# Kernel tuning notes

Measured on AMD Instinct MI355X. Metric: run time of the kernel, lower is better.

The kernel has to match this reference:

```python
import jax, jax.numpy as jnp
import numpy as np

EPS = 1e-5

def conv3d(x, w, b):
    y = jax.lax.conv_general_dilated(x, w, (1, 1, 1), [(1, 1), (1, 1), (1, 1)],
                                     dimension_numbers=('NCDHW', 'OIDHW', 'NCDHW'))
    return y + b[None, :, None, None, None]

def batchnorm(x, g, b):
    # training-mode BN: biased batch statistics over (N, D, H, W)
    m = jnp.mean(x, axis=(0, 2, 3, 4), keepdims=True)
    v = jnp.mean((x - m) ** 2, axis=(0, 2, 3, 4), keepdims=True)
    return (x - m) * jax.lax.rsqrt(v + EPS) * g[None, :, None, None, None] + b[None, :, None, None, None]

def deform_conv3d(x, offset, w, b):
    # x: (B,C,D,H,W); offset: (B, 3*27, D,H,W); w: (O,C,3,3,3)
    B, C, D, H, W = x.shape
    N = 27
    xp = jnp.pad(x, ((0, 0), (0, 0), (1, 1), (1, 1), (1, 1)))
    Dp, Hp, Wp = D + 2, H + 2, W + 2
    off = offset.reshape(B, 3, N, D, H, W)
    kk = jnp.arange(3, dtype=x.dtype) - 1.0  # kernel taps -1,0,1
    kd, kh, kw = [a.reshape(-1) for a in jnp.meshgrid(kk, kk, kk, indexing='ij')]
    # sampling positions in padded coords: p0 (=out idx + pad) + kernel tap + learned offset
    pd = jnp.clip((jnp.arange(D, dtype=x.dtype) + 1.0)[None, None, :, None, None]
                  + kd[None, :, None, None, None] + off[:, 0], 0.0, Dp - 1)
    ph = jnp.clip((jnp.arange(H, dtype=x.dtype) + 1.0)[None, None, None, :, None]
                  + kh[None, :, None, None, None] + off[:, 1], 0.0, Hp - 1)
    pw = jnp.clip((jnp.arange(W, dtype=x.dtype) + 1.0)[None, None, None, None, :]
                  + kw[None, :, None, None, None] + off[:, 2], 0.0, Wp - 1)
    q0d = jnp.clip(jnp.floor(pd), 0, Dp - 2); td = jnp.clip(pd - q0d, 0.0, 1.0)
    q0h = jnp.clip(jnp.floor(ph), 0, Hp - 2); th = jnp.clip(ph - q0h, 0.0, 1.0)
    q0w = jnp.clip(jnp.floor(pw), 0, Wp - 2); tw = jnp.clip(pw - q0w, 0.0, 1.0)
    q0d = q0d.astype(jnp.int32); q0h = q0h.astype(jnp.int32); q0w = q0w.astype(jnp.int32)
    xf = xp.reshape(B, C, -1)
    acc = jnp.zeros((B, C, N, D, H, W), dtype=x.dtype)
    for i in (0, 1):
        for j in (0, 1):
            for k in (0, 1):
                idx = ((q0d + i) * Hp + (q0h + j)) * Wp + (q0w + k)  # (B,N,D,H,W)
                g = ((td if i else 1.0 - td) * (th if j else 1.0 - th) * (tw if k else 1.0 - tw))
                gath = jnp.take_along_axis(xf, idx.reshape(B, 1, -1), axis=2).reshape(B, C, N, D, H, W)
                acc = acc + g[:, None] * gath
    out = jnp.einsum('bcndhw,ocn->bodhw', acc, w.reshape(w.shape[0], C, N))
    return out + b[None, :, None, None, None]


def setup_inputs() -> dict:
    ks = jax.random.split(jax.random.key(0), 16)
    s = 0.05
    f32 = jnp.float32
    return {
        'x': jax.random.normal(ks[0], (4, 1, 28, 28, 8), f32),
        'c1w': jax.random.normal(ks[1], (32, 1, 3, 3, 3), f32) * s, 'c1b': jnp.zeros((32,), f32),
        'g1': jnp.ones((32,), f32), 'b1': jnp.zeros((32,), f32),
        'c2w': jax.random.normal(ks[2], (64, 32, 3, 3, 3), f32) * s, 'c2b': jnp.zeros((64,), f32),
        'g2': jnp.ones((64,), f32), 'b2': jnp.zeros((64,), f32),
        'c3w': jax.random.normal(ks[3], (128, 64, 3, 3, 3), f32) * s, 'c3b': jnp.zeros((128,), f32),
        'g3': jnp.ones((128,), f32), 'b3': jnp.zeros((128,), f32),
        'ow': jax.random.normal(ks[4], (81, 128, 3, 3, 3), f32) * s, 'ob': jnp.zeros((81,), f32),
        'dw': jax.random.normal(ks[5], (128, 128, 3, 3, 3), f32) * s, 'db': jnp.zeros((128,), f32),
        'g4': jnp.ones((128,), f32), 'b4': jnp.zeros((128,), f32),
        'fcw': jax.random.normal(ks[6], (10, 128), f32) * s, 'fcb': jnp.zeros((10,), f32),
    }


def reference(x, c1w, c1b, g1, b1, c2w, c2b, g2, b2, c3w, c3b, g3, b3,
              ow, ob, dw, db, g4, b4, fcw, fcb):
    h = batchnorm(jax.nn.relu(conv3d(x, c1w, c1b)), g1, b1)
    h = batchnorm(jax.nn.relu(conv3d(h, c2w, c2b)), g2, b2)
    h = batchnorm(jax.nn.relu(conv3d(h, c3w, c3b)), g3, b3)
    offsets = conv3d(h, ow, ob)
    h = batchnorm(jax.nn.relu(deform_conv3d(h, offsets, dw, db)), g4, b4)
    pooled = jnp.mean(h, axis=(2, 3, 4))  # avg_pool over full (28,28,d) extent
    logits = pooled @ fcw.T + fcb
    return jax.nn.log_softmax(logits, axis=1), offsets
```

## Files before the change

kernel.cpp:

```cpp
#include <hip/hip_runtime.h>
#include <math.h>

#define BB 4
#define SP 6272
#define NSP 25088
#define EPS 1e-5f

typedef unsigned short u16;
typedef __attribute__((ext_vector_type(8))) short v8s;
typedef __attribute__((ext_vector_type(4))) float v4f;

__device__ __forceinline__ u16 f2b(float f) {
    unsigned u = __float_as_uint(f);
    return (u16)((u + 0x7fffu + ((u >> 16) & 1u)) >> 16);
}
__device__ __forceinline__ float b2f(u16 s) {
    return __uint_as_float(((unsigned)s) << 16);
}
__device__ __forceinline__ float b2f_lo(unsigned x) { return __uint_as_float(x << 16); }
__device__ __forceinline__ float b2f_hi(unsigned x) { return __uint_as_float(x & 0xffff0000u); }

__global__ __launch_bounds__(256) __attribute__((amdgpu_waves_per_eu(1, 4)))
void conv1_shfl(const float* __restrict__ X, const float* __restrict__ Wt,
                const float* __restrict__ bias, u16* __restrict__ Ybf,
                float* __restrict__ s_sum, float* __restrict__ s_sq)
{
    const int OT = 16;
    __shared__ float red[4][32];
    int xblk = blockIdx.x;
    int sblk = (xblk & 7) * 13 + (xblk >> 3);
    if (sblk >= 98) return;
    int t = threadIdx.x;
    int s = sblk * 256 + t;
    int b = s / SP;
    int sp = s - b * SP;
    int d = sp / 224;
    int r = sp - d * 224;
    int h = r >> 3;
    int w = r & 7;
    int o0 = blockIdx.y * OT;

    float mdh[9]; int odh[9];
    #pragma unroll
    for (int i = 0; i < 3; i++) {
        int dd = d + i - 1;
        float md = ((unsigned)dd < 28u) ? 1.f : 0.f;
        int ddc = min(max(dd, 0), 27);
        #pragma unroll
        for (int j = 0; j < 3; j++) {
            int hh = h + j - 1;
            float mh = ((unsigned)hh < 28u) ? 1.f : 0.f;
            int hhc = min(max(hh, 0), 27);
            mdh[i * 3 + j] = md * mh;
            odh[i * 3 + j] = ddc * 224 + hhc * 8 + w;
        }
    }
    float mw0 = (w > 0) ? 1.f : 0.f;
    float mw2 = (w < 7) ? 1.f : 0.f;

    float acc[OT];
    #pragma unroll
    for (int oo = 0; oo < OT; oo++) acc[oo] = bias[o0 + oo];

    const float* xc = X + (size_t)b * SP;
    #pragma unroll
    for (int t9 = 0; t9 < 9; t9++) {
        float x0 = xc[odh[t9]];
        float m = mdh[t9];
        float xm = __shfl_up(x0, 1, 64) * (m * mw0);
        float xz = x0 * m;
        float xp = __shfl_down(x0, 1, 64) * (m * mw2);
        #pragma unroll
        for (int oo = 0; oo < OT; oo++) {
            const float* wp = Wt + (size_t)(o0 + oo) * 27 + t9 * 3;
            acc[oo] = fmaf(xm, wp[0], acc[oo]);
            acc[oo] = fmaf(xz, wp[1], acc[oo]);
            acc[oo] = fmaf(xp, wp[2], acc[oo]);
        }
    }
    float sv[OT];
    #pragma unroll
    for (int oo = 0; oo < OT; oo++) sv[oo] = fmaxf(acc[oo], 0.f);

    unsigned pk[8];
    #pragma unroll
    for (int j = 0; j < 8; j++)
        pk[j] = (unsigned)f2b(sv[2 * j]) | ((unsigned)f2b(sv[2 * j + 1]) << 16);
    u16* row = Ybf + (size_t)(b * SP + sp) * 32 + o0;
    *(uint4*)(row)     = make_uint4(pk[0], pk[1], pk[2], pk[3]);
    *(uint4*)(row + 8) = make_uint4(pk[4], pk[5], pk[6], pk[7]);

    int l = t & 63, wvv = t >> 6;
    #pragma unroll
    for (int oo = 0; oo < OT; oo++) {
        float ss = sv[oo], qv = ss * ss;
        #pragma unroll
        for (int m = 1; m < 64; m <<= 1) {
            ss += __shfl_xor(ss, m, 64);
            qv += __shfl_xor(qv, m, 64);
        }
        if (l == 0) { red[wvv][oo] = ss; red[wvv][16 + oo] = qv; }
    }
    __syncthreads();
    if (t < 32) {
        float tot = red[0][t] + red[1][t] + red[2][t] + red[3][t];
        if (t < 16) atomicAdd(&s_sum[o0 + t], tot);
        else        atomicAdd(&s_sq[o0 + t - 16], tot);
    }
}

__global__ __launch_bounds__(256) void prepack_all(const float* __restrict__ c2w,
        const float* __restrict__ c3w, const float* __restrict__ ow,
        const float* __restrict__ dw, u16* __restrict__ wpk2,
        u16* __restrict__ wpk3, u16* __restrict__ wpko, u16* __restrict__ dwa,
        float* __restrict__ ws0)
{
    int bx = blockIdx.x;
    if (bx >= 4536) {
        int i = (bx - 4536) * 256 + threadIdx.x;
        if (i < 2048) ws0[i] = 0.f;
        return;
    }
    int idx = bx * 256 + threadIdx.x;
    if (idx < 55296) {
        int t = idx / 2048, rem = idx & 2047, o = rem >> 5, c = rem & 31;
        wpk2[idx] = f2b(c2w[((size_t)o * 32 + c) * 27 + t]);
    } else if (idx < 276480) {
        int i = idx - 55296;
        int t = i / 8192, rem = i & 8191, o = rem >> 6, c = rem & 63;
        wpk3[i] = f2b(c3w[((size_t)o * 64 + c) * 27 + t]);
    } else if (idx < 718848) {
        int i = idx - 276480;
        int t = i / 16384, rem = i & 16383, o = rem >> 7, c = rem & 127;
        wpko[i] = f2b((o < 81) ? ow[((size_t)o * 128 + c) * 27 + t] : 0.f);
    } else {
        int i = idx - 718848;
        int j = i & 7, r = (i >> 3) & 15, q = (i >> 7) & 3;
        int kc = (i >> 9) & 3, ot = (i >> 11) & 7, n = i >> 14;
        int o = ot * 16 + r, c = kc * 32 + q * 8 + j;
        dwa[i] = f2b(dw[((size_t)o * 128 + c) * 27 + n]);
    }
}

template<int CIN, int OPAD, bool OFFOUT, bool BNIN>
__global__ __launch_bounds__(256) __attribute__((amdgpu_waves_per_eu(1, 4)))
void conv_mfma(const u16* __restrict__ X, const u16* __restrict__ Wpk,
               const float* __restrict__ bias, u16* __restrict__ Ybf,
               float* __restrict__ offs, float* __restrict__ s_sum,
               float* __restrict__ s_sq, const float* __restrict__ in_sum,
               const float* __restrict__ in_sq, const float* __restrict__ in_g,
               const float* __restrict__ in_b)
{
    const int HS = CIN + 8;
    __shared__ u16 xs[160 * HS];
    __shared__ float scin[BNIN ? CIN : 1], shin[BNIN ? CIN : 1];

    int tid = threadIdx.x;
    int fid = blockIdx.x;
    int g = (fid & 7) * 98 + (fid >> 3);
    int b = g / 196;
    int rem = g - b * 196;
    int d0 = (rem / 14) * 2, h0 = (rem % 14) * 2;

    if (BNIN) {
        if (tid < CIN) {
            float m = in_sum[tid] * (1.f / NSP);
            float v = in_sq[tid] * (1.f / NSP) - m * m;
            float sc = in_g[tid] * rsqrtf(v + EPS);
            scin[tid] = sc;
            shin[tid] = in_b[tid] - m * sc;
        }
        __syncthreads();
    }

    const int NCH = CIN / 8;
    for (int idx = tid; idx < 160 * NCH; idx += 256) {
        int pos = idx / NCH, ch = idx - pos * NCH;
        int dz = pos / 40, r2 = pos - dz * 40;
        int hz = r2 / 10, wz = r2 - hz * 10;
        int dd = d0 + dz - 1, hh = h0 + hz - 1, ww = wz - 1;
        uint4 val = make_uint4(0, 0, 0, 0);
        if ((unsigned)dd < 28u && (unsigned)hh < 28u && (unsigned)ww < 8u) {
            val = *(const uint4*)(X + ((size_t)(b * SP + dd * 224 + hh * 8 + ww) * CIN + ch * 8));
            if (BNIN) {
                int cb = ch * 8;
                float f0 = b2f_lo(val.x) * scin[cb]     + shin[cb];
                float f1 = b2f_hi(val.x) * scin[cb + 1] + shin[cb + 1];
                float f2 = b2f_lo(val.y) * scin[cb + 2] + shin[cb + 2];
                float f3 = b2f_hi(val.y) * scin[cb + 3] + shin[cb + 3];
                float f4 = b2f_lo(val.z) * scin[cb + 4] + shin[cb + 4];
                float f5 = b2f_hi(val.z) * scin[cb + 5] + shin[cb + 5];
                float f6 = b2f_lo(val.w) * scin[cb + 6] + shin[cb + 6];
                float f7 = b2f_hi(val.w) * scin[cb + 7] + shin[cb + 7];
                val.x = (unsigned)f2b(f0) | ((unsigned)f2b(f1) << 16);
                val.y = (unsigned)f2b(f2) | ((unsigned)f2b(f3) << 16);
                val.z = (unsigned)f2b(f4) | ((unsigned)f2b(f5) << 16);
                val.w = (unsigned)f2b(f6) | ((unsigned)f2b(f7) << 16);
            }
        }
        *(uint4*)(xs + pos * HS + ch * 8) = val;
    }
    __syncthreads();

    int l = tid & 63, wv = tid >> 6;
    int q = l >> 4, r = l & 15;
    int hl = r >> 3, wl = r & 7;

    if (OFFOUT && blockIdx.y == 1) {
        int dl = wv >> 1;
        int o = 64 + ((wv & 1) << 4) + r;
        const u16* ap = xs + ((4 + hl + 1) * 10 + wl + 1) * HS + 8 * q + dl * 40 * HS;
        const u16* wp0 = Wpk + (size_t)o * CIN + 8 * q;
        v4f acc = {0.f, 0.f, 0.f, 0.f};
        #pragma unroll
        for (int t = 0; t < 27; t++) {
            const int koff = ((t / 9) - 1) * 40 + (((t / 3) % 3) - 1) * 10 + (t % 3) - 1;
            const u16* wt = wp0 + (size_t)t * OPAD * CIN;
            #pragma unroll
            for (int c0 = 0; c0 < CIN; c0 += 32) {
                v8s a0 = *(const v8s*)(ap + koff * HS + c0);
                v8s bf = *(const v8s*)(wt + c0);
                acc = __builtin_amdgcn_mfma_f32_16x16x32_bf16(a0, bf, acc, 0, 0, 0);
            }
        }
        float bo = (o < 81) ? bias[o] : 0.f;
        #pragma unroll
        for (int rg = 0; rg < 4; rg++) {
            int rowl = q * 4 + rg;
            int sp = (d0 + dl) * 224 + (h0 + (rowl >> 3)) * 8 + (rowl & 7);
            if (o < 81) offs[((size_t)(b * 81 + o)) * SP + sp] = acc[rg] + bo;
        }
        return;
    }

    int o_base = blockIdx.y * 64 + wv * 16;
    int o = o_base + r;

    const u16* a0p = xs + ((4 + hl + 1) * 10 + wl + 1) * HS + 8 * q;
    const u16* a1p = a0p + 40 * HS;
    const u16* wp0 = Wpk + (size_t)o * CIN + 8 * q;

    v4f acc0 = {0.f, 0.f, 0.f, 0.f}, acc1 = {0.f, 0.f, 0.f, 0.f};
    #pragma unroll
    for (int t = 0; t < 27; t++) {
        const int koff = ((t / 9) - 1) * 40 + (((t / 3) % 3) - 1) * 10 + (t % 3) - 1;
        const u16* wt = wp0 + (size_t)t * OPAD * CIN;
        #pragma unroll
        for (int c0 = 0; c0 < CIN; c0 += 32) {
            v8s a0 = *(const v8s*)(a0p + koff * HS + c0);
            v8s a1 = *(const v8s*)(a1p + koff * HS + c0);
            v8s bf = *(const v8s*)(wt + c0);
            acc0 = __builtin_amdgcn_mfma_f32_16x16x32_bf16(a0, bf, acc0, 0, 0, 0);
            acc1 = __builtin_amdgcn_mfma_f32_16x16x32_bf16(a1, bf, acc1, 0, 0, 0);
        }
    }

    if (OFFOUT) {
        float bo = (o < 81) ? bias[o] : 0.f;
        #pragma unroll
        for (int s2 = 0; s2 < 2; s2++) {
            v4f A = s2 ? acc1 : acc0;
            #pragma unroll
            for (int rg = 0; rg < 4; rg++) {
                int rowl = q * 4 + rg;
                int sp = (d0 + s2) * 224 + (h0 + (rowl >> 3)) * 8 + (rowl & 7);
                if (o < 81) offs[((size_t)(b * 81 + o)) * SP + sp] = A[rg] + bo;
            }
        }
    } else {
        float bo = bias[o];
        float rs = 0.f, rq = 0.f;
        #pragma unroll
        for (int s2 = 0; s2 < 2; s2++) {
            v4f A = s2 ? acc1 : acc0;
            #pragma unroll
            for (int rg = 0; rg < 4; rg++) {
                int rowl = q * 4 + rg;
                int sp = (d0 + s2) * 224 + (h0 + (rowl >> 3)) * 8 + (rowl & 7);
                float v = fmaxf(A[rg] + bo, 0.f);
                Ybf[(size_t)(b * SP + sp) * OPAD + o] = f2b(v);
                rs += v; rq += v * v;
            }
        }
        rs += __shfl_xor(rs, 16, 64); rs += __shfl_xor(rs, 32, 64);
        rq += __shfl_xor(rq, 16, 64); rq += __shfl_xor(rq, 32, 64);
        if (l < 16) { atomicAdd(&s_sum[o_base + l], rs); atomicAdd(&s_sq[o_base + l], rq); }
    }
}

template<int C>
__global__ __launch_bounds__(256) void bn_bf(const u16* __restrict__ Y,
        const float* __restrict__ s_sum, const float* __restrict__ s_sq,
        const float* __restrict__ g, const float* __restrict__ bb,
        u16* __restrict__ Xo)
{
    __shared__ float sc_s[C], sh_s[C];
    int t = threadIdx.x;
    if (t < C) {
        float m  = s_sum[t] * (1.f / NSP);
        float v  = s_sq[t] * (1.f / NSP) - m * m;
        float sc = g[t] * rsqrtf(v + EPS);
        sc_s[t] = sc;
        sh_s[t] = bb[t] - m * sc;
    }
    __syncthreads();
    int idx = blockIdx.x * 256 + t;
    uint4 v = ((const uint4*)Y)[idx];
    int cb = (idx & (C / 8 - 1)) * 8;
    float f0 = b2f_lo(v.x) * sc_s[cb]     + sh_s[cb];
    float f1 = b2f_hi(v.x) * sc_s[cb + 1] + sh_s[cb + 1];
    float f2 = b2f_lo(v.y) * sc_s[cb + 2] + sh_s[cb + 2];
    float f3 = b2f_hi(v.y) * sc_s[cb + 3] + sh_s[cb + 3];
    float f4 = b2f_lo(v.z) * sc_s[cb + 4] + sh_s[cb + 4];
    float f5 = b2f_hi(v.z) * sc_s[cb + 5] + sh_s[cb + 5];
    float f6 = b2f_lo(v.w) * sc_s[cb + 6] + sh_s[cb + 6];
    float f7 = b2f_hi(v.w) * sc_s[cb + 7] + sh_s[cb + 7];
    uint4 pk;
    pk.x = (unsigned)f2b(f0) | ((unsigned)f2b(f1) << 16);
    pk.y = (unsigned)f2b(f2) | ((unsigned)f2b(f3) << 16);
    pk.z = (unsigned)f2b(f4) | ((unsigned)f2b(f5) << 16);
    pk.w = (unsigned)f2b(f6) | ((unsigned)f2b(f7) << 16);
    ((uint4*)Xo)[idx] = pk;
}

__global__ __launch_bounds__(256) __attribute__((amdgpu_waves_per_eu(1, 4)))
void deform_pool(const u16* __restrict__ Ht, const float* __restrict__ OFF,
                 const u16* __restrict__ Wa, const float* __restrict__ db,
                 float* __restrict__ pooledraw, float* __restrict__ sumsq4)
{
    __shared__ float offs_lds[81 * 32];
    __shared__ int ig_s[32][8][2];
    __shared__ u16 Vb[32][136];
    __shared__ float reds[128], redq[128];

    int fid = blockIdx.x;
    int xcd = fid & 7;
    int local = fid >> 3;
    if (local >= 98) return;
    int b = xcd >> 1;
    int d = (xcd & 1) * 14 + local / 7;
    int h0 = (local % 7) * 4;

    int t = threadIdx.x;
    if (t < 128) { reds[t] = 0.f; redq[t] = 0.f; }

    int gp = t >> 3, gcr = t & 7;
    int glh = gp >> 3, gw = gp & 7, gh = h0 + glh;
    int co = t & 15, pg = t >> 4;
    int l = t & 63, wv = t >> 6;
    int q = l >> 4, r = l & 15;

    v4f acc[2][2];
    acc[0][0] = (v4f){0.f,0.f,0.f,0.f}; acc[0][1] = (v4f){0.f,0.f,0.f,0.f};
    acc[1][0] = (v4f){0.f,0.f,0.f,0.f}; acc[1][1] = (v4f){0.f,0.f,0.f,0.f};

    const u16* hb = Ht + (size_t)b * SP * 128;

    for (int i = t; i < 2592; i += 256) {
        int ch = i >> 5, p = i & 31;
        offs_lds[i] = OFF[(size_t)b * 81 * SP + (size_t)ch * SP
                          + d * 224 + (h0 + (p >> 3)) * 8 + (p & 7)];
    }

    for (int n = 0; n < 27; n++) {
        __syncthreads();
        {
            int kd = n / 9 - 1, kh = (n / 3) % 3 - 1, kw = n % 3 - 1;
            float od  = offs_lds[n * 32 + gp];
            float oh  = offs_lds[(27 + n) * 32 + gp];
            float owv = offs_lds[(54 + n) * 32 + gp];
            float pd = fminf(fmaxf((float)(d + 1 + kd) + od, 0.f), 29.f);
            float ph = fminf(fmaxf((float)(gh + 1 + kh) + oh, 0.f), 29.f);
            float pw = fminf(fmaxf((float)(gw + 1 + kw) + owv, 0.f), 9.f);
            float qd = fminf(floorf(pd), 28.f);
            float qh = fminf(floorf(ph), 28.f);
            float qw = fminf(floorf(pw), 8.f);
            float td = fminf(pd - qd, 1.f);
            float th = fminf(ph - qh, 1.f);
            float tw = fminf(pw - qw, 1.f);
            int iqd = (int)qd - 1, iqh = (int)qh - 1, iqw = (int)qw - 1;
            int i = gcr >> 2, j = (gcr >> 1) & 1, k = gcr & 1;
            int du = iqd + i, hu = iqh + j, wu = iqw + k;
            bool val = (unsigned)du < 28u && (unsigned)hu < 28u && (unsigned)wu < 8u;
            float gg = (i ? td : 1.f - td) * (j ? th : 1.f - th) * (k ? tw : 1.f - tw);
            ig_s[gp][gcr][0] = val ? (du * 224 + hu * 8 + wu) : 0;
            ig_s[gp][gcr][1] = __float_as_int(val ? gg : 0.f);
        }
        __syncthreads();
        #pragma unroll
        for (int pp = 0; pp < 2; pp++) {
            int p = pg * 2 + pp;
            float va[8] = {0.f,0.f,0.f,0.f,0.f,0.f,0.f,0.f};
            #pragma unroll
            for (int cr = 0; cr < 8; cr++) {
                int2 pr = *(const int2*)&ig_s[p][cr][0];
                float gg = __int_as_float(pr.y);
                uint4 xv = *(const uint4*)(hb + (size_t)pr.x * 128 + co * 8);
                va[0] = fmaf(gg, b2f_lo(xv.x), va[0]);
                va[1] = fmaf(gg, b2f_hi(xv.x), va[1]);
                va[2] = fmaf(gg, b2f_lo(xv.y), va[2]);
                va[3] = fmaf(gg, b2f_hi(xv.y), va[3]);
                va[4] = fmaf(gg, b2f_lo(xv.z), va[4]);
                va[5] = fmaf(gg, b2f_hi(xv.z), va[5]);
                va[6] = fmaf(gg, b2f_lo(xv.w), va[6]);
                va[7] = fmaf(gg, b2f_hi(xv.w), va[7]);
            }
            uint4 pk;
            pk.x = (unsigned)f2b(va[0]) | ((unsigned)f2b(va[1]) << 16);
            pk.y = (unsigned)f2b(va[2]) | ((unsigned)f2b(va[3]) << 16);
            pk.z = (unsigned)f2b(va[4]) | ((unsigned)f2b(va[5]) << 16);
            pk.w = (unsigned)f2b(va[6]) | ((unsigned)f2b(va[7]) << 16);
            *(uint4*)&Vb[p][co * 8] = pk;
        }
        __syncthreads();
        const u16* wn = Wa + (size_t)n * 16384;
        #pragma unroll
        for (int oti = 0; oti < 2; oti++) {
            int ot = wv * 2 + oti;
            #pragma unroll
            for (int kc = 0; kc < 4; kc++) {
                v8s af = *(const v8s*)(wn + ((((ot * 4 + kc) * 4 + q) * 16 + r) * 8));
                v8s bf0 = *(const v8s*)&Vb[r][kc * 32 + q * 8];
                v8s bf1 = *(const v8s*)&Vb[16 + r][kc * 32 + q * 8];
                acc[oti][0] = __builtin_amdgcn_mfma_f32_16x16x32_bf16(af, bf0, acc[oti][0], 0, 0, 0);
                acc[oti][1] = __builtin_amdgcn_mfma_f32_16x16x32_bf16(af, bf1, acc[oti][1], 0, 0, 0);
            }
        }
    }

    #pragma unroll
    for (int oti = 0; oti < 2; oti++) {
        #pragma unroll
        for (int rg = 0; rg < 4; rg++) {
            int o = (wv * 2 + oti) * 16 + q * 4 + rg;
            float bo = db[o];
            float v0 = fmaxf(acc[oti][0][rg] + bo, 0.f);
            float v1 = fmaxf(acc[oti][1][rg] + bo, 0.f);
            float s = v0 + v1, qq = v0 * v0 + v1 * v1;
            s += __shfl_xor(s, 1, 64);  qq += __shfl_xor(qq, 1, 64);
            s += __shfl_xor(s, 2, 64);  qq += __shfl_xor(qq, 2, 64);
            s += __shfl_xor(s, 4, 64);  qq += __shfl_xor(qq, 4, 64);
            s += __shfl_xor(s, 8, 64);  qq += __shfl_xor(qq, 8, 64);
            if (r == 0) { atomicAdd(&reds[o], s); atomicAdd(&redq[o], qq); }
        }
    }
    __syncthreads();
    if (t < 128) {
        atomicAdd(&pooledraw[b * 128 + t], reds[t]);
        atomicAdd(&sumsq4[t], redq[t]);
    }
}

__global__ __launch_bounds__(256) void final_head_emit(const float* __restrict__ pooledraw,
        const float* __restrict__ sumsq4, const float* __restrict__ g4,
        const float* __restrict__ b4, const float* __restrict__ fcw,
        const float* __restrict__ fcb, float* __restrict__ out)
{
    int t = threadIdx.x;
    __shared__ float pooled_s[4][128];
    __shared__ float logits[4][10];
    if (t < 128) {
        float s0 = pooledraw[t], s1 = pooledraw[128 + t];
        float s2 = pooledraw[256 + t], s3 = pooledraw[384 + t];
        float tot = s0 + s1 + s2 + s3;
        float m  = tot * (1.f / NSP);
        float v  = sumsq4[t] * (1.f / NSP) - m * m;
        float sc = g4[t] * rsqrtf(v + EPS);
        float sh = b4[t] - m * sc;
        pooled_s[0][t] = s0 * (1.f / SP) * sc + sh;
        pooled_s[1][t] = s1 * (1.f / SP) * sc + sh;
        pooled_s[2][t] = s2 * (1.f / SP) * sc + sh;
        pooled_s[3][t] = s3 * (1.f / SP) * sc + sh;
    }
    __syncthreads();
    if (t < 40) {
        int b = t / 10, j = t % 10;
        float l = fcb[j];
        for (int c = 0; c < 128; c++) l = fmaf(pooled_s[b][c], fcw[j * 128 + c], l);
        logits[b][j] = l;
    }
    __syncthreads();
    if (t < 4) {
        float mx = -1e30f;
        for (int j = 0; j < 10; j++) mx = fmaxf(mx, logits[t][j]);
        float se = 0.f;
        for (int j = 0; j < 10; j++) se += expf(logits[t][j] - mx);
        float lse = mx + logf(se);
        for (int j = 0; j < 10; j++) out[t * 10 + j] = logits[t][j] - lse;
    }
}

extern "C" void kernel_launch(void* const* d_in, const int* in_sizes, int n_in,
                              void* d_out, int out_size, void* d_ws, size_t ws_size,
                              hipStream_t stream)
{
    (void)in_sizes; (void)n_in; (void)out_size; (void)ws_size;
    const float* x   = (const float*)d_in[0];
    const float* c1w = (const float*)d_in[1];
    const float* c1b = (const float*)d_in[2];
    const float* g1  = (const float*)d_in[3];
    const float* b1  = (const float*)d_in[4];
    const float* c2w = (const float*)d_in[5];
    const float* c2b = (const float*)d_in[6];
    const float* g2  = (const float*)d_in[7];
    const float* b2  = (const float*)d_in[8];
    const float* c3w = (const float*)d_in[9];
    const float* c3b = (const float*)d_in[10];
    const float* g3  = (const float*)d_in[11];
    const float* b3  = (const float*)d_in[12];
    const float* ow  = (const float*)d_in[13];
    const float* ob  = (const float*)d_in[14];
    const float* dw  = (const float*)d_in[15];
    const float* db  = (const float*)d_in[16];
    const float* g4  = (const float*)d_in[17];
    const float* b4  = (const float*)d_in[18];
    const float* fcw = (const float*)d_in[19];
    const float* fcb = (const float*)d_in[20];

    float* ws = (float*)d_ws;
    float* S1 = ws + 0,   *Q1 = ws + 32;
    float* S2 = ws + 64,  *Q2 = ws + 128;
    float* S3 = ws + 192, *Q3 = ws + 320;
    float* PO = ws + 448;
    float* Q4 = ws + 960;
    u16* y1bf = (u16*)(ws + 2048);
    u16* y2bf = y1bf + 802816;
    u16* y3bf = y2bf + 1605632;
    u16* x3bf = y3bf + 3211264;
    u16* wpk2 = x3bf + 3211264;
    u16* wpk3 = wpk2 + 55296;
    u16* wpko = wpk3 + 221184;
    u16* dwa  = wpko + 442368;

    float* outf = (float*)d_out;
    float* offp = outf + 40;

    prepack_all<<<4544, 256, 0, stream>>>(c2w, c3w, ow, dw, wpk2, wpk3, wpko, dwa, ws);

    conv1_shfl<<<dim3(104, 2), 256, 0, stream>>>(x, c1w, c1b, y1bf, S1, Q1);

    conv_mfma<32, 64, false, true><<<dim3(784, 1), 256, 0, stream>>>(
        y1bf, wpk2, c2b, y2bf, nullptr, S2, Q2, S1, Q1, g1, b1);

    conv_mfma<64, 128, false, true><<<dim3(784, 2), 256, 0, stream>>>(
        y2bf, wpk3, c3b, y3bf, nullptr, S3, Q3, S2, Q2, g2, b2);

    bn_bf<128><<<1568, 256, 0, stream>>>(y3bf, S3, Q3, g3, b3, x3bf);

    conv_mfma<128, 128, true, false><<<dim3(784, 2), 256, 0, stream>>>(
        x3bf, wpko, ob, nullptr, offp, nullptr, nullptr, nullptr, nullptr, nullptr, nullptr);
    deform_pool<<<800, 256, 0, stream>>>(x3bf, offp, dwa, db, PO, Q4);
    final_head_emit<<<1, 256, 0, stream>>>(PO, Q4, g4, b4, fcw, fcb, outf);
}
```

Before: 417.5 us.

## Widen conv3 and offset-conv tiles to cover all output channels per block

The conv3 and offset-conv launches previously split output channels across two grid-y blocks, and each of those blocks re-staged the same input halo tile into LDS. Now one block computes all output channels: conv3 has each wave do 2x2 MFMA tiles, and the offset conv has each wave do three 16-channel tiles. This halves the grid and the redundant staging and BN-input work, at the cost of more accumulator registers and possibly lower occupancy. Separately, the manual bf16 round-and-pack is replaced with the HIP __float22bfloat162_rn intrinsic, which may lower to a packed conversion instruction.

```diff
diff --git a/kernel.cpp b/kernel.cpp
--- a/kernel.cpp
+++ b/kernel.cpp
@@ -1,4 +1,5 @@
 #include <hip/hip_runtime.h>
+#include <hip/hip_bf16.h>
 #include <math.h>
 
 #define BB 4
@@ -19,6 +20,12 @@
 }
 __device__ __forceinline__ float b2f_lo(unsigned x) { return __uint_as_float(x << 16); }
 __device__ __forceinline__ float b2f_hi(unsigned x) { return __uint_as_float(x & 0xffff0000u); }
+__device__ __forceinline__ unsigned pk2(float a, float b) {
+    __hip_bfloat162 h = __float22bfloat162_rn(make_float2(a, b));
+    unsigned u;
+    __builtin_memcpy(&u, &h, 4);
+    return u;
+}
 
 __global__ __launch_bounds__(256) __attribute__((amdgpu_waves_per_eu(1, 4)))
 void conv1_shfl(const float* __restrict__ X, const float* __restrict__ Wt,
@@ -84,8 +91,7 @@
 
     unsigned pk[8];
     #pragma unroll
-    for (int j = 0; j < 8; j++)
-        pk[j] = (unsigned)f2b(sv[2 * j]) | ((unsigned)f2b(sv[2 * j + 1]) << 16);
+    for (int j = 0; j < 8; j++) pk[j] = pk2(sv[2 * j], sv[2 * j + 1]);
     u16* row = Ybf + (size_t)(b * SP + sp) * 32 + o0;
     *(uint4*)(row)     = make_uint4(pk[0], pk[1], pk[2], pk[3]);
     *(uint4*)(row + 8) = make_uint4(pk[4], pk[5], pk[6], pk[7]);
@@ -142,7 +148,7 @@
     }
 }
 
-template<int CIN, int OPAD, bool OFFOUT, bool BNIN>
+template<int CIN, int OPAD, bool OFFOUT, bool BNIN, bool WIDE>
 __global__ __launch_bounds__(256) __attribute__((amdgpu_waves_per_eu(1, 4)))
 void conv_mfma(const u16* __restrict__ X, const u16* __restrict__ Wpk,
                const float* __restrict__ bias, u16* __restrict__ Ybf,
@@ -192,10 +198,8 @@
                 float f5 = b2f_hi(val.z) * scin[cb + 5] + shin[cb + 5];
                 float f6 = b2f_lo(val.w) * scin[cb + 6] + shin[cb + 6];
                 float f7 = b2f_hi(val.w) * scin[cb + 7] + shin[cb + 7];
-                val.x = (unsigned)f2b(f0) | ((unsigned)f2b(f1) << 16);
-                val.y = (unsigned)f2b(f2) | ((unsigned)f2b(f3) << 16);
-                val.z = (unsigned)f2b(f4) | ((unsigned)f2b(f5) << 16);
-                val.w = (unsigned)f2b(f6) | ((unsigned)f2b(f7) << 16);
+                val.x = pk2(f0, f1); val.y = pk2(f2, f3);
+                val.z = pk2(f4, f5); val.w = pk2(f6, f7);
             }
         }
         *(uint4*)(xs + pos * HS + ch * 8) = val;
@@ -206,38 +210,99 @@
     int q = l >> 4, r = l & 15;
     int hl = r >> 3, wl = r & 7;
 
-    if (OFFOUT && blockIdx.y == 1) {
+    if (OFFOUT) {
         int dl = wv >> 1;
-        int o = 64 + ((wv & 1) << 4) + r;
+        int ot0 = (wv & 1) * 3;
         const u16* ap = xs + ((4 + hl + 1) * 10 + wl + 1) * HS + 8 * q + dl * 40 * HS;
+        int o0 = ot0 * 16 + r;
+        const u16* wpA = Wpk + (size_t)o0 * CIN + 8 * q;
+        v4f acc[3];
+        acc[0] = (v4f){0.f,0.f,0.f,0.f};
+        acc[1] = (v4f){0.f,0.f,0.f,0.f};
+        acc[2] = (v4f){0.f,0.f,0.f,0.f};
+        #pragma unroll
+        for (int t = 0; t < 27; t++) {
+            const int koff = ((t / 9) - 1) * 40 + (((t / 3) % 3) - 1) * 10 + (t % 3) - 1;
+            const u16* wt = wpA + (size_t)t * OPAD * CIN;
+            #pragma unroll
+            for (int c0 = 0; c0 < CIN; c0 += 32) {
+                v8s a0 = *(const v8s*)(ap + koff * HS + c0);
+                v8s b0 = *(const v8s*)(wt + c0);
+                v8s b1 = *(const v8s*)(wt + 16 * CIN + c0);
+                v8s b2 = *(const v8s*)(wt + 32 * CIN + c0);
+                acc[0] = __builtin_amdgcn_mfma_f32_16x16x32_bf16(a0, b0, acc[0], 0, 0, 0);
+                acc[1] = __builtin_amdgcn_mfma_f32_16x16x32_bf16(a0, b1, acc[1], 0, 0, 0);
+                acc[2] = __builtin_amdgcn_mfma_f32_16x16x32_bf16(a0, b2, acc[2], 0, 0, 0);
+            }
+        }
+        #pragma unroll
+        for (int j = 0; j < 3; j++) {
+            int o = o0 + 16 * j;
+            if (o < 81) {
+                float bo = bias[o];
+                #pragma unroll
+                for (int rg = 0; rg < 4; rg++) {
+                    int rowl = q * 4 + rg;
+                    int sp = (d0 + dl) * 224 + (h0 + (rowl >> 3)) * 8 + (rowl & 7);
+                    offs[((size_t)(b * 81 + o)) * SP + sp] = acc[j][rg] + bo;
+                }
+            }
+        }
+        return;
+    }
+
+    const u16* a0p = xs + ((4 + hl + 1) * 10 + wl + 1) * HS + 8 * q;
+    const u16* a1p = a0p + 40 * HS;
+
+    if (WIDE) {
+        int o = wv * 16 + r;
         const u16* wp0 = Wpk + (size_t)o * CIN + 8 * q;
-        v4f acc = {0.f, 0.f, 0.f, 0.f};
+        v4f acc[2][2];
+        acc[0][0] = (v4f){0.f,0.f,0.f,0.f}; acc[0][1] = (v4f){0.f,0.f,0.f,0.f};
+        acc[1][0] = (v4f){0.f,0.f,0.f,0.f}; acc[1][1] = (v4f){0.f,0.f,0.f,0.f};
         #pragma unroll
         for (int t = 0; t < 27; t++) {
             const int koff = ((t / 9) - 1) * 40 + (((t / 3) % 3) - 1) * 10 + (t % 3) - 1;
             const u16* wt = wp0 + (size_t)t * OPAD * CIN;
             #pragma unroll
             for (int c0 = 0; c0 < CIN; c0 += 32) {
-                v8s a0 = *(const v8s*)(ap + koff * HS + c0);
-                v8s bf = *(const v8s*)(wt + c0);
-                acc = __builtin_amdgcn_mfma_f32_16x16x32_bf16(a0, bf, acc, 0, 0, 0);
-            }
-        }
-        float bo = (o < 81) ? bias[o] : 0.f;
-        #pragma unroll
-        for (int rg = 0; rg < 4; rg++) {
-            int rowl = q * 4 + rg;
-            int sp = (d0 + dl) * 224 + (h0 + (rowl >> 3)) * 8 + (rowl & 7);
-            if (o < 81) offs[((size_t)(b * 81 + o)) * SP + sp] = acc[rg] + bo;
+                v8s a0 = *(const v8s*)(a0p + koff * HS + c0);
+                v8s a1 = *(const v8s*)(a1p + koff * HS + c0);
+                v8s b0 = *(const v8s*)(wt + c0);
+                v8s b1 = *(const v8s*)(wt + 64 * CIN + c0);
+                acc[0][0] = __builtin_amdgcn_mfma_f32_16x16x32_bf16(a0, b0, acc[0][0], 0, 0, 0);
+                acc[0][1] = __builtin_amdgcn_mfma_f32_16x16x32_bf16(a1, b0, acc[0][1], 0, 0, 0);
+                acc[1][0] = __builtin_amdgcn_mfma_f32_16x16x32_bf16(a0, b1, acc[1][0], 0, 0, 0);
+                acc[1][1] = __builtin_amdgcn_mfma_f32_16x16x32_bf16(a1, b1, acc[1][1], 0, 0, 0);
+            }
+        }
+        #pragma unroll
+        for (int oti = 0; oti < 2; oti++) {
+            int o_base = wv * 16 + oti * 64;
+            int oo = o_base + r;
+            float bo = bias[oo];
+            float rs = 0.f, rq = 0.f;
+            #pragma unroll
+            for (int s2 = 0; s2 < 2; s2++) {
+                v4f A = acc[oti][s2];
+                #pragma unroll
+                for (int rg = 0; rg < 4; rg++) {
+                    int rowl = q * 4 + rg;
+                    int sp = (d0 + s2) * 224 + (h0 + (rowl >> 3)) * 8 + (rowl & 7);
+                    float v = fmaxf(A[rg] + bo, 0.f);
+                    Ybf[(size_t)(b * SP + sp) * OPAD + oo] = f2b(v);
+                    rs += v; rq += v * v;
+                }
+            }
+            rs += __shfl_xor(rs, 16, 64); rs += __shfl_xor(rs, 32, 64);
+            rq += __shfl_xor(rq, 16, 64); rq += __shfl_xor(rq, 32, 64);
+            if (l < 16) { atomicAdd(&s_sum[o_base + l], rs); atomicAdd(&s_sq[o_base + l], rq); }
         }
         return;
     }
 
     int o_base = blockIdx.y * 64 + wv * 16;
     int o = o_base + r;
-
-    const u16* a0p = xs + ((4 + hl + 1) * 10 + wl + 1) * HS + 8 * q;
-    const u16* a1p = a0p + 40 * HS;
     const u16* wp0 = Wpk + (size_t)o * CIN + 8 * q;
 
     v4f acc0 = {0.f, 0.f, 0.f, 0.f}, acc1 = {0.f, 0.f, 0.f, 0.f};
@@ -255,19 +320,7 @@
         }
     }
 
-    if (OFFOUT) {
-        float bo = (o < 81) ? bias[o] : 0.f;
-        #pragma unroll
-        for (int s2 = 0; s2 < 2; s2++) {
-            v4f A = s2 ? acc1 : acc0;
-            #pragma unroll
-            for (int rg = 0; rg < 4; rg++) {
-                int rowl = q * 4 + rg;
-                int sp = (d0 + s2) * 224 + (h0 + (rowl >> 3)) * 8 + (rowl & 7);
-                if (o < 81) offs[((size_t)(b * 81 + o)) * SP + sp] = A[rg] + bo;
-            }
-        }
-    } else {
+    {
         float bo = bias[o];
         float rs = 0.f, rq = 0.f;
         #pragma unroll
@@ -316,10 +369,8 @@
     float f6 = b2f_lo(v.w) * sc_s[cb + 6] + sh_s[cb + 6];
     float f7 = b2f_hi(v.w) * sc_s[cb + 7] + sh_s[cb + 7];
     uint4 pk;
-    pk.x = (unsigned)f2b(f0) | ((unsigned)f2b(f1) << 16);
-    pk.y = (unsigned)f2b(f2) | ((unsigned)f2b(f3) << 16);
-    pk.z = (unsigned)f2b(f4) | ((unsigned)f2b(f5) << 16);
-    pk.w = (unsigned)f2b(f6) | ((unsigned)f2b(f7) << 16);
+    pk.x = pk2(f0, f1); pk.y = pk2(f2, f3);
+    pk.z = pk2(f4, f5); pk.w = pk2(f6, f7);
     ((uint4*)Xo)[idx] = pk;
 }
 
@@ -406,10 +457,8 @@
                 va[7] = fmaf(gg, b2f_hi(xv.w), va[7]);
             }
             uint4 pk;
-            pk.x = (unsigned)f2b(va[0]) | ((unsigned)f2b(va[1]) << 16);
-            pk.y = (unsigned)f2b(va[2]) | ((unsigned)f2b(va[3]) << 16);
-            pk.z = (unsigned)f2b(va[4]) | ((unsigned)f2b(va[5]) << 16);
-            pk.w = (unsigned)f2b(va[6]) | ((unsigned)f2b(va[7]) << 16);
+            pk.x = pk2(va[0], va[1]); pk.y = pk2(va[2], va[3]);
+            pk.z = pk2(va[4], va[5]); pk.w = pk2(va[6], va[7]);
             *(uint4*)&Vb[p][co * 8] = pk;
         }
         __syncthreads();
@@ -539,16 +588,17 @@
 
     conv1_shfl<<<dim3(104, 2), 256, 0, stream>>>(x, c1w, c1b, y1bf, S1, Q1);
 
-    conv_mfma<32, 64, false, true><<<dim3(784, 1), 256, 0, stream>>>(
+    conv_mfma<32, 64, false, true, false><<<dim3(784, 1), 256, 0, stream>>>(
         y1bf, wpk2, c2b, y2bf, nullptr, S2, Q2, S1, Q1, g1, b1);
 
-    conv_mfma<64, 128, false, true><<<dim3(784, 2), 256, 0, stream>>>(
+    conv_mfma<64, 128, false, true, true><<<dim3(784, 1), 256, 0, stream>>>(
         y2bf, wpk3, c3b, y3bf, nullptr, S3, Q3, S2, Q2, g2, b2);
 
     bn_bf<128><<<1568, 256, 0, stream>>>(y3bf, S3, Q3, g3, b3, x3bf);
 
-    conv_mfma<128, 128, true, false><<<dim3(784, 2), 256, 0, stream>>>(
+    conv_mfma<128, 128, true, false, false><<<dim3(784, 1), 256, 0, stream>>>(
         x3bf, wpko, ob, nullptr, offp, nullptr, nullptr, nullptr, nullptr, nullptr, nullptr);
+
     deform_pool<<<800, 256, 0, stream>>>(x3bf, offp, dwa, db, PO, Q4);
     final_head_emit<<<1, 256, 0, stream>>>(PO, Q4, g4, b4, fcw, fcb, outf);
 }
```

New measurement: 460.3 us. 10.3% more time.
